# Performance work log

Measured on AMD Instinct MI355X. Metric: run time of the kernel, lower is better.

The kernel has to match this reference:

```python
import jax, jax.numpy as jnp
import numpy as np

V, E, H, L = 512, 128, 256, 4
B, T = 128, 1024


def setup_inputs() -> dict:
    key = jax.random.key(0)
    ks = jax.random.split(key, 16)
    s = 0.05
    inp = {
        "x": jax.random.randint(ks[0], (B, T), 0, V),
        "tags": jax.random.randint(ks[1], (B, T), 0, L),
        "mask": jnp.ones((B, T), dtype=bool),
        "emb": jax.random.normal(ks[2], (V, E), jnp.float32) * s,
        "w_ih_f": jax.random.normal(ks[3], (3 * H, E), jnp.float32) * s,
        "w_hh_f": jax.random.normal(ks[4], (3 * H, H), jnp.float32) * s,
        "b_ih_f": jax.random.normal(ks[5], (3 * H,), jnp.float32) * s,
        "b_hh_f": jax.random.normal(ks[6], (3 * H,), jnp.float32) * s,
        "w_ih_b": jax.random.normal(ks[7], (3 * H, E), jnp.float32) * s,
        "w_hh_b": jax.random.normal(ks[8], (3 * H, H), jnp.float32) * s,
        "b_ih_b": jax.random.normal(ks[9], (3 * H,), jnp.float32) * s,
        "b_hh_b": jax.random.normal(ks[10], (3 * H,), jnp.float32) * s,
        "fc_w": jax.random.normal(ks[11], (L, 2 * H), jnp.float32) * s,
        "fc_b": jax.random.normal(ks[12], (L,), jnp.float32) * s,
        "start_trans": jax.random.normal(ks[13], (L,), jnp.float32) * 0.1,
        "end_trans": jax.random.normal(ks[14], (L,), jnp.float32) * 0.1,
        "trans": jax.random.normal(ks[15], (L, L), jnp.float32) * 0.1,
    }
    return inp


def _gru_scan(xe, w_ih, w_hh, b_ih, b_hh):
    # xe: [B,T,E] -> out [B,T,H]; PyTorch GRU gate order: r, z, n
    gi = jnp.einsum("bte,ge->btg", xe, w_ih) + b_ih  # [B,T,3H]
    gi = jnp.swapaxes(gi, 0, 1)  # [T,B,3H]
    h0 = jnp.zeros((xe.shape[0], H), xe.dtype)

    def step(h, gi_t):
        gh = h @ w_hh.T + b_hh
        i_r, i_z, i_n = jnp.split(gi_t, 3, axis=-1)
        h_r, h_z, h_n = jnp.split(gh, 3, axis=-1)
        r = jax.nn.sigmoid(i_r + h_r)
        z = jax.nn.sigmoid(i_z + h_z)
        n = jnp.tanh(i_n + r * h_n)
        h_new = (1.0 - z) * n + z * h
        return h_new, h_new

    _, out = jax.lax.scan(step, h0, gi)
    return jnp.swapaxes(out, 0, 1)  # [B,T,H]


def _crf_neg_llh(emissions, tags, mask, start_trans, end_trans, trans):
    # emissions [B,T,L], tags [B,T] int, mask [B,T] bool
    maskf = mask.astype(emissions.dtype)
    # ----- numerator: score of gold path -----
    em_sel = jnp.take_along_axis(emissions, tags[..., None], axis=2)[..., 0]  # [B,T]
    trans_sel = trans[tags[:, :-1], tags[:, 1:]]  # [B,T-1]
    score = start_trans[tags[:, 0]] + em_sel[:, 0]
    score = score + jnp.sum((trans_sel + em_sel[:, 1:]) * maskf[:, 1:], axis=1)
    seq_ends = jnp.sum(mask.astype(jnp.int32), axis=1) - 1  # [B]
    last_tags = jnp.take_along_axis(tags, seq_ends[:, None], axis=1)[:, 0]
    score = score + end_trans[last_tags]
    # ----- denominator: forward algorithm (logsumexp scan) -----
    alpha0 = start_trans[None, :] + emissions[:, 0]  # [B,L]
    em_rest = jnp.swapaxes(emissions[:, 1:], 0, 1)  # [T-1,B,L]
    m_rest = jnp.swapaxes(mask[:, 1:], 0, 1)  # [T-1,B]

    def step(alpha, inputs):
        emit_t, m_t = inputs
        nxt = jax.nn.logsumexp(alpha[:, :, None] + trans[None] + emit_t[:, None, :], axis=1)
        alpha = jnp.where(m_t[:, None], nxt, alpha)
        return alpha, None

    alpha, _ = jax.lax.scan(step, alpha0, (em_rest, m_rest))
    logZ = jax.nn.logsumexp(alpha + end_trans[None, :], axis=1)  # [B]
    llh = score - logZ
    return -jnp.mean(llh)  # reduction='mean', negated in Segmenter.forward


def reference(x, tags, mask, emb, w_ih_f, w_hh_f, b_ih_f, b_hh_f,
              w_ih_b, w_hh_b, b_ih_b, b_hh_b, fc_w, fc_b,
              start_trans, end_trans, trans):
    xe = emb[x]  # [B,T,E]
    out_f = _gru_scan(xe, w_ih_f, w_hh_f, b_ih_f, b_hh_f)
    out_b = _gru_scan(xe[:, ::-1], w_ih_b, w_hh_b, b_ih_b, b_hh_b)[:, ::-1]
    gru_out = jnp.concatenate([out_f, out_b], axis=-1)  # [B,T,2H]
    emissions = jnp.einsum("bth,lh->btl", gru_out, fc_w) + fc_b  # [B,T,L]
    return _crf_neg_llh(emissions, tags, mask, start_trans, end_trans, trans)
```

## Files before the change

kernel.cpp:

```cpp
#include <hip/hip_runtime.h>
#include <hip/hip_fp16.h>

#define Tn 1024
#define NB 128
#define WPAD 260

typedef _Float16 h2_t __attribute__((ext_vector_type(2)));

__device__ __forceinline__ float dot2f(h2_t a, h2_t b, float c) {
#if __has_builtin(__builtin_amdgcn_fdot2)
  return __builtin_amdgcn_fdot2(a, b, c, false);
#else
  return c + (float)a[0] * (float)b[0] + (float)a[1] * (float)b[1];
#endif
}

__device__ __forceinline__ h2_t u2h(unsigned u) {
  union { unsigned u; h2_t h; } c; c.u = u; return c.h;
}

__global__ __launch_bounds__(768)
void gv_build(const float* __restrict__ emb,
              const float* __restrict__ wihf, const float* __restrict__ bihf,
              const float* __restrict__ wihb, const float* __restrict__ bihb,
              float* __restrict__ gv)
{
  const int d  = blockIdx.x >> 7;
  const int v4 = (blockIdx.x & 127) * 4;
  const float* wih = d ? wihb : wihf;
  const float* bih = d ? bihb : bihf;
  __shared__ float se[4][128];
  const int tid = threadIdx.x;
  if (tid < 512) se[tid >> 7][tid & 127] = emb[(v4 + (tid >> 7)) * 128 + (tid & 127)];
  __syncthreads();
  const int row = tid;
  const float b0 = bih[row];
  float a0 = b0, a1 = b0, a2 = b0, a3 = b0;
  #pragma unroll
  for (int e = 0; e < 128; e += 4) {
    const float4 w = *reinterpret_cast<const float4*>(&wih[row * 128 + e]);
    a0 = fmaf(w.x, se[0][e], a0); a0 = fmaf(w.y, se[0][e+1], a0);
    a0 = fmaf(w.z, se[0][e+2], a0); a0 = fmaf(w.w, se[0][e+3], a0);
    a1 = fmaf(w.x, se[1][e], a1); a1 = fmaf(w.y, se[1][e+1], a1);
    a1 = fmaf(w.z, se[1][e+2], a1); a1 = fmaf(w.w, se[1][e+3], a1);
    a2 = fmaf(w.x, se[2][e], a2); a2 = fmaf(w.y, se[2][e+1], a2);
    a2 = fmaf(w.z, se[2][e+2], a2); a2 = fmaf(w.w, se[2][e+3], a2);
    a3 = fmaf(w.x, se[3][e], a3); a3 = fmaf(w.y, se[3][e+1], a3);
    a3 = fmaf(w.z, se[3][e+2], a3); a3 = fmaf(w.w, se[3][e+3], a3);
  }
  float* out = gv + (size_t)(d * 512 + v4) * 768 + row;
  out[0] = a0; out[768] = a1; out[1536] = a2; out[2304] = a3;
}

__global__ __launch_bounds__(512, 2)
void gru_scan(const int* __restrict__ x,
              const float* __restrict__ gv,
              const float* __restrict__ whhf,
              const float* __restrict__ whhb,
              const float* __restrict__ bhhf,
              const float* __restrict__ bhhb,
              const float* __restrict__ fcw,
              float* __restrict__ em)
{
  const int tid  = threadIdx.x;
  const int j    = tid >> 1;
  const int half = tid & 1;
  const int dir  = blockIdx.x & 1;
  const int b    = blockIdx.x >> 1;

  const float* whh = dir ? whhb : whhf;
  const float* bhh = dir ? bhhb : bhhf;

  __shared__ float wstage[64 * WPAD];
  __shared__ __align__(16) _Float16 hbuf[2][256];

  h2_t wr[64], wz[64], wn[64];

  for (int ch = 0; ch < 12; ++ch) {
    const int r0 = ch * 64;
    #pragma unroll
    for (int i = 0; i < 8; ++i) {
      const int f  = (i * 512 + tid) * 4;
      const int rr = f >> 8;
      const int cc = f & 255;
      *reinterpret_cast<float4*>(&wstage[rr * WPAD + cc]) =
          *reinterpret_cast<const float4*>(&whh[(r0 + rr) * 256 + cc]);
    }
    __syncthreads();
    #pragma unroll
    for (int g = 0; g < 3; ++g) {
      const int row = j + g * 256;
      if (row >= r0 && row < r0 + 64) {
        const float* src = &wstage[(row - r0) * WPAD + half * 128];
        #pragma unroll
        for (int kk = 0; kk < 64; ++kk) {
          const float2 wv = *reinterpret_cast<const float2*>(&src[2 * kk]);
          h2_t w; w[0] = (_Float16)wv.x; w[1] = (_Float16)wv.y;
          if (g == 0) wr[kk] = w;
          else if (g == 1) wz[kk] = w;
          else wn[kk] = w;
        }
      }
    }
    __syncthreads();
  }

  float br = 0.f, bz = 0.f, bn = 0.f;
  if (half == 0) { br = bhh[j]; bz = bhh[j + 256]; bn = bhh[j + 512]; }

  const int el    = tid & 3;
  const int ec    = (tid >> 2) & 15;
  const int wv_id = tid >> 6;
  h2_t fc2[8];
  #pragma unroll
  for (int m = 0; m < 8; ++m) {
    const int cbase = el * 512 + dir * 256 + ec * 16 + 2 * m;
    fc2[m][0] = (_Float16)fcw[cbase];
    fc2[m][1] = (_Float16)fcw[cbase + 1];
  }

  if (tid < 256) hbuf[0][tid] = (_Float16)0.f;
  float ho = 0.f;
  __syncthreads();

  const int* xb  = x + b * Tn;
  float*     emo = em + (dir * NB + b) * Tn * 4;

  for (int step = 0; step < Tn; ++step) {
    const int cur = step & 1;
    const int tt  = dir ? (Tn - 1 - step) : step;

    const int tok = xb[tt];
    float gir = 0.f, giz = 0.f, gin = 0.f;
    if (half == 0) {
      const float* g = gv + (dir * 512 + tok) * 768;
      gir = g[j]; giz = g[j + 256]; gin = g[j + 512];
    }

    if (wv_id == (step & 7) && step > 0) {
      const int ptt = dir ? (Tn - step) : (step - 1);
      const uint4* hq4 = reinterpret_cast<const uint4*>(&hbuf[cur][0]) + ec * 2;
      const uint4 q0 = hq4[0];
      const uint4 q1 = hq4[1];
      float acc = 0.f;
      acc = dot2f(fc2[0], u2h(q0.x), acc);
      acc = dot2f(fc2[1], u2h(q0.y), acc);
      acc = dot2f(fc2[2], u2h(q0.z), acc);
      acc = dot2f(fc2[3], u2h(q0.w), acc);
      acc = dot2f(fc2[4], u2h(q1.x), acc);
      acc = dot2f(fc2[5], u2h(q1.y), acc);
      acc = dot2f(fc2[6], u2h(q1.z), acc);
      acc = dot2f(fc2[7], u2h(q1.w), acc);
      acc += __shfl_xor(acc, 4);
      acc += __shfl_xor(acc, 8);
      acc += __shfl_xor(acc, 16);
      acc += __shfl_xor(acc, 32);
      if (ec == 0) emo[ptt * 4 + el] = acc;
    }

    float dr = 0.f, dz = 0.f, dn = 0.f;
    const uint4* hv4 = reinterpret_cast<const uint4*>(&hbuf[cur][half * 128]);
    #pragma unroll
    for (int q = 0; q < 16; ++q) {
      const uint4 hq = hv4[q];
      const h2_t h0 = u2h(hq.x), h1 = u2h(hq.y), h2v = u2h(hq.z), h3 = u2h(hq.w);
      dr = dot2f(wr[4*q+0], h0, dr);  dz = dot2f(wz[4*q+0], h0, dz);  dn = dot2f(wn[4*q+0], h0, dn);
      dr = dot2f(wr[4*q+1], h1, dr);  dz = dot2f(wz[4*q+1], h1, dz);  dn = dot2f(wn[4*q+1], h1, dn);
      dr = dot2f(wr[4*q+2], h2v, dr); dz = dot2f(wz[4*q+2], h2v, dz); dn = dot2f(wn[4*q+2], h2v, dn);
      dr = dot2f(wr[4*q+3], h3, dr);  dz = dot2f(wz[4*q+3], h3, dz);  dn = dot2f(wn[4*q+3], h3, dn);
    }

    const float pr = __shfl_xor(dr, 1);
    const float pz = __shfl_xor(dz, 1);
    const float pn = __shfl_xor(dn, 1);

    if (half == 0) {
      const float ghr = dr + pr + br;
      const float ghz = dz + pz + bz;
      const float ghn = dn + pn + bn;
      const float r = 1.f / (1.f + __expf(-(gir + ghr)));
      const float z = 1.f / (1.f + __expf(-(giz + ghz)));
      const float npre = gin + r * ghn;
      const float e2 = __expf(-2.f * npre);
      const float n = (1.f - e2) / (1.f + e2);
      const float hnew = (1.f - z) * n + z * ho;
      ho = hnew;
      hbuf[cur ^ 1][j] = (_Float16)hnew;
    }
    __syncthreads();
  }

  if (wv_id == 0) {
    const int ptt = dir ? 0 : (Tn - 1);
    const uint4* hq4 = reinterpret_cast<const uint4*>(&hbuf[Tn & 1][0]) + ec * 2;
    const uint4 q0 = hq4[0];
    const uint4 q1 = hq4[1];
    float acc = 0.f;
    acc = dot2f(fc2[0], u2h(q0.x), acc);
    acc = dot2f(fc2[1], u2h(q0.y), acc);
    acc = dot2f(fc2[2], u2h(q0.z), acc);
    acc = dot2f(fc2[3], u2h(q0.w), acc);
    acc = dot2f(fc2[4], u2h(q1.x), acc);
    acc = dot2f(fc2[5], u2h(q1.y), acc);
    acc = dot2f(fc2[6], u2h(q1.z), acc);
    acc = dot2f(fc2[7], u2h(q1.w), acc);
    acc += __shfl_xor(acc, 4);
    acc += __shfl_xor(acc, 8);
    acc += __shfl_xor(acc, 16);
    acc += __shfl_xor(acc, 32);
    if (ec == 0) emo[ptt * 4 + el] = acc;
  }
}

__global__ __launch_bounds__(64)
void crf_nllh(const int* __restrict__ tags,
              const float* __restrict__ em,
              const float* __restrict__ fc_b,
              const float* __restrict__ st,
              const float* __restrict__ et,
              const float* __restrict__ tr,
              float* __restrict__ llh)
{
  const int lane = threadIdx.x;
  const int l = lane & 3;
  const int q = lane >> 2;
  const int b = blockIdx.x * 16 + q;
  const float* ef = em + (size_t)b * Tn * 4;
  const float* eb = em + ((size_t)NB + b) * Tn * 4;
  const int* tg = tags + b * Tn;
  const float fcb = fc_b[l];
  const float tc0 = tr[l * 4 + l];
  const float tc1 = tr[(l ^ 1) * 4 + l];
  const float tc2 = tr[(l ^ 2) * 4 + l];
  const float tc3 = tr[(l ^ 3) * 4 + l];

  const float e0 = ef[l] + eb[l] + fcb;
  float alpha = st[l] + e0;
  int tprev = tg[0];
  float score = (tprev == l) ? (st[l] + e0) : 0.f;

  #pragma unroll 8
  for (int t = 1; t < Tn; ++t) {
    const float e = ef[t * 4 + l] + eb[t * 4 + l] + fcb;
    const int tc = tg[t];
    if (tc == l) {
      const int s2 = tprev ^ l;
      const float tsel = (s2 & 1) ? ((s2 & 2) ? tc3 : tc1)
                                  : ((s2 & 2) ? tc2 : tc0);
      score += e + tsel;
    }
    tprev = tc;
    const float a1 = __shfl_xor(alpha, 1);
    const float a2 = __shfl_xor(alpha, 2);
    const float a3 = __shfl_xor(alpha, 3);
    const float v0 = alpha + tc0;
    const float v1 = a1 + tc1;
    const float v2 = a2 + tc2;
    const float v3 = a3 + tc3;
    const float mx = fmaxf(fmaxf(v0, v1), fmaxf(v2, v3));
    const float s = __expf(v0 - mx) + __expf(v1 - mx) + __expf(v2 - mx) + __expf(v3 - mx);
    alpha = mx + __logf(s) + e;
  }

  score += (tprev == l) ? et[l] : 0.f;
  float ae = alpha + et[l];
  float m1 = fmaxf(ae, __shfl_xor(ae, 1));
  m1 = fmaxf(m1, __shfl_xor(m1, 2));
  float se = __expf(ae - m1);
  se += __shfl_xor(se, 1);
  se += __shfl_xor(se, 2);
  const float logZ = m1 + __logf(se);
  float sc = score + __shfl_xor(score, 1);
  sc += __shfl_xor(sc, 2);
  if (l == 0) llh[b] = sc - logZ;
}

__global__ __launch_bounds__(128)
void reduce_mean(const float* __restrict__ llh, float* __restrict__ out)
{
  const int t = threadIdx.x;
  float v = llh[t];
  #pragma unroll
  for (int m = 32; m >= 1; m >>= 1) v += __shfl_xor(v, m);
  __shared__ float s2[2];
  if ((t & 63) == 0) s2[t >> 6] = v;
  __syncthreads();
  if (t == 0) out[0] = -(s2[0] + s2[1]) * (1.f / 128.f);
}

extern "C" void kernel_launch(void* const* d_in, const int* in_sizes, int n_in,
                              void* d_out, int out_size, void* d_ws, size_t ws_size,
                              hipStream_t stream) {
  const int*   x    = (const int*)d_in[0];
  const int*   tags = (const int*)d_in[1];
  const float* emb  = (const float*)d_in[3];
  const float* wihf = (const float*)d_in[4];
  const float* whhf = (const float*)d_in[5];
  const float* bihf = (const float*)d_in[6];
  const float* bhhf = (const float*)d_in[7];
  const float* wihb = (const float*)d_in[8];
  const float* whhb = (const float*)d_in[9];
  const float* bihb = (const float*)d_in[10];
  const float* bhhb = (const float*)d_in[11];
  const float* fcw  = (const float*)d_in[12];
  const float* fcb  = (const float*)d_in[13];
  const float* st   = (const float*)d_in[14];
  const float* et   = (const float*)d_in[15];
  const float* tr   = (const float*)d_in[16];

  char* ws = (char*)d_ws;
  float* gv  = (float*)ws;
  float* em  = (float*)(ws + 3145728);
  float* llh = (float*)(ws + 3145728 + 4194304);

  gv_build<<<dim3(256), dim3(768), 0, stream>>>(emb, wihf, bihf, wihb, bihb, gv);
  gru_scan<<<dim3(256), dim3(512), 0, stream>>>(x, gv, whhf, whhb, bhhf, bhhb, fcw, em);
  crf_nllh<<<dim3(8), dim3(64), 0, stream>>>(tags, em, fcb, st, et, tr, llh);
  reduce_mean<<<dim3(1), dim3(128), 0, stream>>>(llh, (float*)d_out);
}
```

Baseline: 1.512 ms.

## Split each GRU hidden unit across four lanes with 1024-thread blocks and DPP reductions

```diff
diff --git a/kernel.cpp b/kernel.cpp
--- a/kernel.cpp
+++ b/kernel.cpp
@@ -3,7 +3,6 @@
 
 #define Tn 1024
 #define NB 128
-#define WPAD 260
 
 typedef _Float16 h2_t __attribute__((ext_vector_type(2)));
 
@@ -17,6 +16,15 @@
 
 __device__ __forceinline__ h2_t u2h(unsigned u) {
   union { unsigned u; h2_t h; } c; c.u = u; return c.h;
+}
+
+__device__ __forceinline__ float dpp_xor1(float v) {
+  int i = __builtin_bit_cast(int, v);
+  return __builtin_bit_cast(float, __builtin_amdgcn_update_dpp(i, i, 0xB1, 0xF, 0xF, true));
+}
+__device__ __forceinline__ float dpp_xor2(float v) {
+  int i = __builtin_bit_cast(int, v);
+  return __builtin_bit_cast(float, __builtin_amdgcn_update_dpp(i, i, 0x4E, 0xF, 0xF, true));
 }
 
 __global__ __launch_bounds__(768)
@@ -52,7 +60,7 @@
   out[0] = a0; out[768] = a1; out[1536] = a2; out[2304] = a3;
 }
 
-__global__ __launch_bounds__(512, 2)
+__global__ __launch_bounds__(1024)
 void gru_scan(const int* __restrict__ x,
               const float* __restrict__ gv,
               const float* __restrict__ whhf,
@@ -62,95 +70,95 @@
               const float* __restrict__ fcw,
               float* __restrict__ em)
 {
-  const int tid  = threadIdx.x;
-  const int j    = tid >> 1;
-  const int half = tid & 1;
-  const int dir  = blockIdx.x & 1;
-  const int b    = blockIdx.x >> 1;
+  const int tid = threadIdx.x;
+  const int j   = tid >> 2;
+  const int q   = tid & 3;
+  const int dir = blockIdx.x & 1;
+  const int b   = blockIdx.x >> 1;
 
   const float* whh = dir ? whhb : whhf;
   const float* bhh = dir ? bhhb : bhhf;
 
-  __shared__ float wstage[64 * WPAD];
-  __shared__ __align__(16) _Float16 hbuf[2][256];
-
-  h2_t wr[64], wz[64], wn[64];
-
-  for (int ch = 0; ch < 12; ++ch) {
-    const int r0 = ch * 64;
+  __shared__ float wstage[128][260];
+  __shared__ __align__(16) char hb[2 * 576];
+  __shared__ __align__(16) h2_t fcs[4][132];
+
+  if (tid < 512) {
+    const int l = tid >> 7, c = tid & 127;
+    h2_t f;
+    f[0] = (_Float16)fcw[l * 512 + dir * 256 + 2 * c];
+    f[1] = (_Float16)fcw[l * 512 + dir * 256 + 2 * c + 1];
+    fcs[l][c] = f;
+  }
+  if (tid < 72) *reinterpret_cast<uint4*>(hb + tid * 16) = make_uint4(0, 0, 0, 0);
+
+  h2_t w[96];
+  for (int ch = 0; ch < 6; ++ch) {
+    const int r0 = ch << 7;
     #pragma unroll
     for (int i = 0; i < 8; ++i) {
-      const int f  = (i * 512 + tid) * 4;
-      const int rr = f >> 8;
-      const int cc = f & 255;
-      *reinterpret_cast<float4*>(&wstage[rr * WPAD + cc]) =
-          *reinterpret_cast<const float4*>(&whh[(r0 + rr) * 256 + cc]);
+      const int f  = i * 1024 + tid;
+      const int rr = f >> 6;
+      const int cc = (f & 63) << 2;
+      *reinterpret_cast<float4*>(&wstage[rr][cc]) =
+          *reinterpret_cast<const float4*>(&whh[(size_t)(r0 + rr) * 256 + cc]);
     }
     __syncthreads();
     #pragma unroll
     for (int g = 0; g < 3; ++g) {
-      const int row = j + g * 256;
-      if (row >= r0 && row < r0 + 64) {
-        const float* src = &wstage[(row - r0) * WPAD + half * 128];
+      const int row = (g << 8) + j;
+      if (row >= r0 && row < r0 + 128) {
+        const float* src = &wstage[row - r0][q << 6];
         #pragma unroll
-        for (int kk = 0; kk < 64; ++kk) {
-          const float2 wv = *reinterpret_cast<const float2*>(&src[2 * kk]);
-          h2_t w; w[0] = (_Float16)wv.x; w[1] = (_Float16)wv.y;
-          if (g == 0) wr[kk] = w;
-          else if (g == 1) wz[kk] = w;
-          else wn[kk] = w;
+        for (int kk = 0; kk < 32; ++kk) {
+          const float2 wv = *reinterpret_cast<const float2*>(src + 2 * kk);
+          h2_t ww; ww[0] = (_Float16)wv.x; ww[1] = (_Float16)wv.y;
+          w[(g << 5) + kk] = ww;
         }
       }
     }
     __syncthreads();
   }
 
-  float br = 0.f, bz = 0.f, bn = 0.f;
-  if (half == 0) { br = bhh[j]; bz = bhh[j + 256]; bn = bhh[j + 512]; }
-
-  const int el    = tid & 3;
-  const int ec    = (tid >> 2) & 15;
-  const int wv_id = tid >> 6;
-  h2_t fc2[8];
-  #pragma unroll
-  for (int m = 0; m < 8; ++m) {
-    const int cbase = el * 512 + dir * 256 + ec * 16 + 2 * m;
-    fc2[m][0] = (_Float16)fcw[cbase];
-    fc2[m][1] = (_Float16)fcw[cbase + 1];
-  }
-
-  if (tid < 256) hbuf[0][tid] = (_Float16)0.f;
-  float ho = 0.f;
-  __syncthreads();
-
-  const int* xb  = x + b * Tn;
-  float*     emo = em + (dir * NB + b) * Tn * 4;
+  float br = 0.f, bz = 0.f, bn = 0.f, ho = 0.f;
+  if (q == 0) { br = bhh[j]; bz = bhh[j + 256]; bn = bhh[j + 512]; }
+
+  const float* gvd  = gv + (size_t)dir * (512 * 768);
+  const int*   xb   = x + b * Tn;
+  float*       emo  = em + (size_t)(dir * NB + b) * (Tn * 4);
+  const int    wv_id = tid >> 6;
+  const int    el    = tid & 3;
+  const int    ec    = (tid >> 2) & 15;
+  const int    hq_off = q * 144;
+  const int    hw_off = (j >> 6) * 144 + (j & 63) * 2;
 
   for (int step = 0; step < Tn; ++step) {
     const int cur = step & 1;
     const int tt  = dir ? (Tn - 1 - step) : step;
-
     const int tok = xb[tt];
+
     float gir = 0.f, giz = 0.f, gin = 0.f;
-    if (half == 0) {
-      const float* g = gv + (dir * 512 + tok) * 768;
-      gir = g[j]; giz = g[j + 256]; gin = g[j + 512];
-    }
-
-    if (wv_id == (step & 7) && step > 0) {
+    if (q == 0) {
+      const float* g = gvd + tok * 768 + j;
+      gir = g[0]; giz = g[256]; gin = g[512];
+    }
+
+    if (wv_id == (step & 15) && step > 0) {
       const int ptt = dir ? (Tn - step) : (step - 1);
-      const uint4* hq4 = reinterpret_cast<const uint4*>(&hbuf[cur][0]) + ec * 2;
-      const uint4 q0 = hq4[0];
-      const uint4 q1 = hq4[1];
+      const char* hp = hb + cur * 576 + (ec >> 2) * 144 + (ec & 3) * 32;
+      const uint4 hA = *reinterpret_cast<const uint4*>(hp);
+      const uint4 hB = *reinterpret_cast<const uint4*>(hp + 16);
+      const uint4 fA = *reinterpret_cast<const uint4*>(&fcs[el][ec * 8]);
+      const uint4 fB = *reinterpret_cast<const uint4*>(&fcs[el][ec * 8 + 4]);
       float acc = 0.f;
-      acc = dot2f(fc2[0], u2h(q0.x), acc);
-      acc = dot2f(fc2[1], u2h(q0.y), acc);
-      acc = dot2f(fc2[2], u2h(q0.z), acc);
-      acc = dot2f(fc2[3], u2h(q0.w), acc);
-      acc = dot2f(fc2[4], u2h(q1.x), acc);
-      acc = dot2f(fc2[5], u2h(q1.y), acc);
-      acc = dot2f(fc2[6], u2h(q1.z), acc);
-      acc = dot2f(fc2[7], u2h(q1.w), acc);
+      acc = dot2f(u2h(fA.x), u2h(hA.x), acc);
+      acc = dot2f(u2h(fA.y), u2h(hA.y), acc);
+      acc = dot2f(u2h(fA.z), u2h(hA.z), acc);
+      acc = dot2f(u2h(fA.w), u2h(hA.w), acc);
+      acc = dot2f(u2h(fB.x), u2h(hB.x), acc);
+      acc = dot2f(u2h(fB.y), u2h(hB.y), acc);
+      acc = dot2f(u2h(fB.z), u2h(hB.z), acc);
+      acc = dot2f(u2h(fB.w), u2h(hB.w), acc);
       acc += __shfl_xor(acc, 4);
       acc += __shfl_xor(acc, 8);
       acc += __shfl_xor(acc, 16);
@@ -159,51 +167,50 @@
     }
 
     float dr = 0.f, dz = 0.f, dn = 0.f;
-    const uint4* hv4 = reinterpret_cast<const uint4*>(&hbuf[cur][half * 128]);
+    const char* hbase = hb + cur * 576 + hq_off;
     #pragma unroll
-    for (int q = 0; q < 16; ++q) {
-      const uint4 hq = hv4[q];
+    for (int c = 0; c < 8; ++c) {
+      const uint4 hq = *reinterpret_cast<const uint4*>(hbase + c * 16);
       const h2_t h0 = u2h(hq.x), h1 = u2h(hq.y), h2v = u2h(hq.z), h3 = u2h(hq.w);
-      dr = dot2f(wr[4*q+0], h0, dr);  dz = dot2f(wz[4*q+0], h0, dz);  dn = dot2f(wn[4*q+0], h0, dn);
-      dr = dot2f(wr[4*q+1], h1, dr);  dz = dot2f(wz[4*q+1], h1, dz);  dn = dot2f(wn[4*q+1], h1, dn);
-      dr = dot2f(wr[4*q+2], h2v, dr); dz = dot2f(wz[4*q+2], h2v, dz); dn = dot2f(wn[4*q+2], h2v, dn);
-      dr = dot2f(wr[4*q+3], h3, dr);  dz = dot2f(wz[4*q+3], h3, dz);  dn = dot2f(wn[4*q+3], h3, dn);
-    }
-
-    const float pr = __shfl_xor(dr, 1);
-    const float pz = __shfl_xor(dz, 1);
-    const float pn = __shfl_xor(dn, 1);
-
-    if (half == 0) {
-      const float ghr = dr + pr + br;
-      const float ghz = dz + pz + bz;
-      const float ghn = dn + pn + bn;
-      const float r = 1.f / (1.f + __expf(-(gir + ghr)));
-      const float z = 1.f / (1.f + __expf(-(giz + ghz)));
-      const float npre = gin + r * ghn;
-      const float e2 = __expf(-2.f * npre);
-      const float n = (1.f - e2) / (1.f + e2);
+      dr = dot2f(w[4*c+0], h0, dr);  dz = dot2f(w[32+4*c+0], h0, dz);  dn = dot2f(w[64+4*c+0], h0, dn);
+      dr = dot2f(w[4*c+1], h1, dr);  dz = dot2f(w[32+4*c+1], h1, dz);  dn = dot2f(w[64+4*c+1], h1, dn);
+      dr = dot2f(w[4*c+2], h2v, dr); dz = dot2f(w[32+4*c+2], h2v, dz); dn = dot2f(w[64+4*c+2], h2v, dn);
+      dr = dot2f(w[4*c+3], h3, dr);  dz = dot2f(w[32+4*c+3], h3, dz);  dn = dot2f(w[64+4*c+3], h3, dn);
+    }
+
+    dr += dpp_xor1(dr); dr += dpp_xor2(dr);
+    dz += dpp_xor1(dz); dz += dpp_xor2(dz);
+    dn += dpp_xor1(dn); dn += dpp_xor2(dn);
+
+    if (q == 0) {
+      const float r    = 1.f / (1.f + __expf(-(gir + dr + br)));
+      const float z    = 1.f / (1.f + __expf(-(giz + dz + bz)));
+      const float npre = gin + r * (dn + bn);
+      const float e2   = __expf(-2.f * npre);
+      const float n    = (1.f - e2) / (1.f + e2);
       const float hnew = (1.f - z) * n + z * ho;
       ho = hnew;
-      hbuf[cur ^ 1][j] = (_Float16)hnew;
+      *reinterpret_cast<_Float16*>(hb + (cur ^ 1) * 576 + hw_off) = (_Float16)hnew;
     }
     __syncthreads();
   }
 
   if (wv_id == 0) {
     const int ptt = dir ? 0 : (Tn - 1);
-    const uint4* hq4 = reinterpret_cast<const uint4*>(&hbuf[Tn & 1][0]) + ec * 2;
-    const uint4 q0 = hq4[0];
-    const uint4 q1 = hq4[1];
+    const char* hp = hb + (Tn & 1) * 576 + (ec >> 2) * 144 + (ec & 3) * 32;
+    const uint4 hA = *reinterpret_cast<const uint4*>(hp);
+    const uint4 hB = *reinterpret_cast<const uint4*>(hp + 16);
+    const uint4 fA = *reinterpret_cast<const uint4*>(&fcs[el][ec * 8]);
+    const uint4 fB = *reinterpret_cast<const uint4*>(&fcs[el][ec * 8 + 4]);
     float acc = 0.f;
-    acc = dot2f(fc2[0], u2h(q0.x), acc);
-    acc = dot2f(fc2[1], u2h(q0.y), acc);
-    acc = dot2f(fc2[2], u2h(q0.z), acc);
-    acc = dot2f(fc2[3], u2h(q0.w), acc);
-    acc = dot2f(fc2[4], u2h(q1.x), acc);
-    acc = dot2f(fc2[5], u2h(q1.y), acc);
-    acc = dot2f(fc2[6], u2h(q1.z), acc);
-    acc = dot2f(fc2[7], u2h(q1.w), acc);
+    acc = dot2f(u2h(fA.x), u2h(hA.x), acc);
+    acc = dot2f(u2h(fA.y), u2h(hA.y), acc);
+    acc = dot2f(u2h(fA.z), u2h(hA.z), acc);
+    acc = dot2f(u2h(fA.w), u2h(hA.w), acc);
+    acc = dot2f(u2h(fB.x), u2h(hB.x), acc);
+    acc = dot2f(u2h(fB.y), u2h(hB.y), acc);
+    acc = dot2f(u2h(fB.z), u2h(hB.z), acc);
+    acc = dot2f(u2h(fB.w), u2h(hB.w), acc);
     acc += __shfl_xor(acc, 4);
     acc += __shfl_xor(acc, 8);
     acc += __shfl_xor(acc, 16);
@@ -314,7 +321,7 @@
   float* llh = (float*)(ws + 3145728 + 4194304);
 
   gv_build<<<dim3(256), dim3(768), 0, stream>>>(emb, wihf, bihf, wihb, bihb, gv);
-  gru_scan<<<dim3(256), dim3(512), 0, stream>>>(x, gv, whhf, whhb, bhhf, bhhb, fcw, em);
+  gru_scan<<<dim3(256), dim3(1024), 0, stream>>>(x, gv, whhf, whhb, bhhf, bhhb, fcw, em);
   crf_nllh<<<dim3(8), dim3(64), 0, stream>>>(tags, em, fcb, st, et, tr, llh);
   reduce_mean<<<dim3(1), dim3(128), 0, stream>>>(llh, (float*)d_out);
 }
```

New measurement: 2.256 ms. 1.49x slower.

## Batch 16 sequences per block and compute GRU recurrence with MFMA

Applied to the files above, without the earlier changes.

```diff
diff --git a/kernel.cpp b/kernel.cpp
--- a/kernel.cpp
+++ b/kernel.cpp
@@ -3,37 +3,30 @@
 
 #define Tn 1024
 #define NB 128
-#define WPAD 260
-
-typedef _Float16 h2_t __attribute__((ext_vector_type(2)));
-
-__device__ __forceinline__ float dot2f(h2_t a, h2_t b, float c) {
-#if __has_builtin(__builtin_amdgcn_fdot2)
-  return __builtin_amdgcn_fdot2(a, b, c, false);
-#else
-  return c + (float)a[0] * (float)b[0] + (float)a[1] * (float)b[1];
-#endif
-}
-
-__device__ __forceinline__ h2_t u2h(unsigned u) {
-  union { unsigned u; h2_t h; } c; c.u = u; return c.h;
-}
+
+#define S_RZ (-1.4426950408889634f)
+#define S_N  (-2.8853900817779268f)
+
+typedef _Float16 f16x8 __attribute__((ext_vector_type(8)));
+typedef _Float16 f16x4 __attribute__((ext_vector_type(4)));
+typedef float    f32x4 __attribute__((ext_vector_type(4)));
 
 __global__ __launch_bounds__(768)
 void gv_build(const float* __restrict__ emb,
-              const float* __restrict__ wihf, const float* __restrict__ bihf,
-              const float* __restrict__ wihb, const float* __restrict__ bihb,
-              float* __restrict__ gv)
+              const float* __restrict__ wihf, const float* __restrict__ bihf, const float* __restrict__ bhhf,
+              const float* __restrict__ wihb, const float* __restrict__ bihb, const float* __restrict__ bhhb,
+              _Float16* __restrict__ gv2)
 {
   const int d  = blockIdx.x >> 7;
   const int v4 = (blockIdx.x & 127) * 4;
   const float* wih = d ? wihb : wihf;
   const float* bih = d ? bihb : bihf;
+  const float* bhh = d ? bhhb : bhhf;
   __shared__ float se[4][128];
   const int tid = threadIdx.x;
   if (tid < 512) se[tid >> 7][tid & 127] = emb[(v4 + (tid >> 7)) * 128 + (tid & 127)];
   __syncthreads();
-  const int row = tid;
+  const int row = tid, g = row >> 8, j = row & 255;
   const float b0 = bih[row];
   float a0 = b0, a1 = b0, a2 = b0, a3 = b0;
   #pragma unroll
@@ -48,167 +41,163 @@
     a3 = fmaf(w.x, se[3][e], a3); a3 = fmaf(w.y, se[3][e+1], a3);
     a3 = fmaf(w.z, se[3][e+2], a3); a3 = fmaf(w.w, se[3][e+3], a3);
   }
-  float* out = gv + (size_t)(d * 512 + v4) * 768 + row;
-  out[0] = a0; out[768] = a1; out[1536] = a2; out[2304] = a3;
+  const float sc  = (g == 2) ? S_N : S_RZ;
+  const float add = (g < 2) ? bhh[row] : 0.f;
+  _Float16* base = gv2 + ((size_t)(d * 512 + v4) * 64 + (j >> 2)) * 16 + g * 4 + (j & 3);
+  base[0]    = (_Float16)(sc * (a0 + add));
+  base[1024] = (_Float16)(sc * (a1 + add));
+  base[2048] = (_Float16)(sc * (a2 + add));
+  base[3072] = (_Float16)(sc * (a3 + add));
+  if (g == 2) {
+    const _Float16 bv = (_Float16)(S_N * bhh[row]);
+    _Float16* bb = gv2 + ((size_t)(d * 512 + v4) * 64 + (j >> 2)) * 16 + 12 + (j & 3);
+    bb[0] = bv; bb[1024] = bv; bb[2048] = bv; bb[3072] = bv;
+  }
 }
 
 __global__ __launch_bounds__(512, 2)
 void gru_scan(const int* __restrict__ x,
-              const float* __restrict__ gv,
+              const _Float16* __restrict__ gv2,
               const float* __restrict__ whhf,
               const float* __restrict__ whhb,
-              const float* __restrict__ bhhf,
-              const float* __restrict__ bhhb,
               const float* __restrict__ fcw,
               float* __restrict__ em)
 {
-  const int tid  = threadIdx.x;
-  const int j    = tid >> 1;
-  const int half = tid & 1;
-  const int dir  = blockIdx.x & 1;
-  const int b    = blockIdx.x >> 1;
+  const int tid = threadIdx.x;
+  const int w   = tid >> 6;
+  const int l   = tid & 63;
+  const int m   = l & 15;
+  const int q   = l >> 4;
+  const int dir = blockIdx.x & 1;
+  const int b0  = (blockIdx.x >> 1) * 16;
 
   const float* whh = dir ? whhb : whhf;
-  const float* bhh = dir ? bhhb : bhhf;
-
-  __shared__ float wstage[64 * WPAD];
-  __shared__ __align__(16) _Float16 hbuf[2][256];
-
-  h2_t wr[64], wz[64], wn[64];
-
-  for (int ch = 0; ch < 12; ++ch) {
-    const int r0 = ch * 64;
-    #pragma unroll
-    for (int i = 0; i < 8; ++i) {
-      const int f  = (i * 512 + tid) * 4;
-      const int rr = f >> 8;
-      const int cc = f & 255;
-      *reinterpret_cast<float4*>(&wstage[rr * WPAD + cc]) =
-          *reinterpret_cast<const float4*>(&whh[(r0 + rr) * 256 + cc]);
+
+  __shared__ _Float16 hls[2][16][264];
+  __shared__ _Float16 emf[8][512];
+
+  for (int i = tid; i < 2 * 16 * 264; i += 512) (&hls[0][0][0])[i] = (_Float16)0.f;
+
+  if (w == 7) {
+    #pragma unroll
+    for (int ks = 0; ks < 8; ++ks) {
+      f16x8 f;
+      #pragma unroll
+      for (int e = 0; e < 8; ++e) {
+        float v = (m < 4) ? fcw[m * 512 + dir * 256 + ks * 32 + q * 8 + e] : 0.f;
+        f[e] = (_Float16)v;
+      }
+      *reinterpret_cast<f16x8*>(&emf[ks][l * 8]) = f;
+    }
+  }
+
+  f16x8 af[2][3][8];
+  #pragma unroll
+  for (int blk = 0; blk < 2; ++blk) {
+    #pragma unroll
+    for (int g = 0; g < 3; ++g) {
+      const int row = g * 256 + (w + 8 * blk) * 16 + m;
+      const float sc = (g == 2) ? S_N : S_RZ;
+      const float* wrow = whh + (size_t)row * 256 + q * 8;
+      #pragma unroll
+      for (int ks = 0; ks < 8; ++ks) {
+        const float4 c0 = *reinterpret_cast<const float4*>(wrow + ks * 32);
+        const float4 c1 = *reinterpret_cast<const float4*>(wrow + ks * 32 + 4);
+        f16x8 f;
+        f[0] = (_Float16)(c0.x * sc); f[1] = (_Float16)(c0.y * sc);
+        f[2] = (_Float16)(c0.z * sc); f[3] = (_Float16)(c0.w * sc);
+        f[4] = (_Float16)(c1.x * sc); f[5] = (_Float16)(c1.y * sc);
+        f[6] = (_Float16)(c1.z * sc); f[7] = (_Float16)(c1.w * sc);
+        af[blk][g][ks] = f;
+      }
+    }
+  }
+  __syncthreads();
+
+  const int*      xrow = x + (size_t)(b0 + m) * Tn;
+  const _Float16* gvd  = gv2 + (size_t)dir * 512 * 1024;
+  float*          emo  = em + (size_t)(dir * NB + b0 + m) * (Tn * 4);
+
+  int tok = xrow[dir ? (Tn - 1) : 0];
+
+  for (int t = 0; t < Tn; ++t) {
+    const int cur = t & 1;
+    const _Float16* hc = &hls[cur][0][0];
+    _Float16*       hn = &hls[cur ^ 1][0][0];
+
+    const _Float16* gp0 = gvd + (size_t)tok * 1024 + ((w + 0) * 4 + q) * 16;
+    const _Float16* gp1 = gvd + (size_t)tok * 1024 + ((w + 8) * 4 + q) * 16;
+    const f16x8 rz0 = *reinterpret_cast<const f16x8*>(gp0);
+    const f16x8 nb0 = *reinterpret_cast<const f16x8*>(gp0 + 8);
+    const f16x8 rz1 = *reinterpret_cast<const f16x8*>(gp1);
+    const f16x8 nb1 = *reinterpret_cast<const f16x8*>(gp1 + 8);
+    if (t + 1 < Tn) tok = xrow[dir ? (Tn - 2 - t) : (t + 1)];
+
+    const f16x4 ho0 = *reinterpret_cast<const f16x4*>(hc + m * 264 + (w + 0) * 16 + q * 4);
+    const f16x4 ho1 = *reinterpret_cast<const f16x4*>(hc + m * 264 + (w + 8) * 16 + q * 4);
+
+    f32x4 acc[2][3] = {{{0,0,0,0},{0,0,0,0},{0,0,0,0}},{{0,0,0,0},{0,0,0,0},{0,0,0,0}}};
+    f32x4 acce = {0,0,0,0};
+    #pragma unroll
+    for (int ks = 0; ks < 8; ++ks) {
+      const f16x8 b = *reinterpret_cast<const f16x8*>(hc + m * 264 + ks * 32 + q * 8);
+      #pragma unroll
+      for (int blk = 0; blk < 2; ++blk) {
+        acc[blk][0] = __builtin_amdgcn_mfma_f32_16x16x32_f16(af[blk][0][ks], b, acc[blk][0], 0, 0, 0);
+        acc[blk][1] = __builtin_amdgcn_mfma_f32_16x16x32_f16(af[blk][1][ks], b, acc[blk][1], 0, 0, 0);
+        acc[blk][2] = __builtin_amdgcn_mfma_f32_16x16x32_f16(af[blk][2][ks], b, acc[blk][2], 0, 0, 0);
+      }
+      if (w == 7) {
+        const f16x8 ef = *reinterpret_cast<const f16x8*>(&emf[ks][l * 8]);
+        acce = __builtin_amdgcn_mfma_f32_16x16x32_f16(ef, b, acce, 0, 0, 0);
+      }
+    }
+
+    if (w == 7 && t > 0 && l < 16) {
+      const int ptt = dir ? (Tn - t) : (t - 1);
+      *reinterpret_cast<f32x4*>(emo + (size_t)ptt * 4) = acce;
+    }
+
+    #pragma unroll
+    for (int blk = 0; blk < 2; ++blk) {
+      const f16x8 rzv = blk ? rz1 : rz0;
+      const f16x8 nbv = blk ? nb1 : nb0;
+      const f16x4 hov = blk ? ho1 : ho0;
+      f16x4 hnv;
+      #pragma unroll
+      for (int r4 = 0; r4 < 4; ++r4) {
+        const float aR = acc[blk][0][r4], aZ = acc[blk][1][r4], aN = acc[blk][2][r4];
+        const float pr = aR + (float)rzv[r4];
+        const float er = __builtin_amdgcn_exp2f(pr);
+        const float rr = __builtin_amdgcn_rcpf(1.f + er);
+        const float pz = aZ + (float)rzv[4 + r4];
+        const float ez = __builtin_amdgcn_exp2f(pz);
+        const float zz = __builtin_amdgcn_rcpf(1.f + ez);
+        float y = fmaf(rr, aN + (float)nbv[4 + r4], (float)nbv[r4]);
+        y = fminf(y, 60.f);
+        const float en = __builtin_amdgcn_exp2f(y);
+        const float nn = (1.f - en) * __builtin_amdgcn_rcpf(1.f + en);
+        const float hv = fmaf(zz, (float)hov[r4] - nn, nn);
+        hnv[r4] = (_Float16)hv;
+      }
+      *reinterpret_cast<f16x4*>(hn + m * 264 + (w + 8 * blk) * 16 + q * 4) = hnv;
     }
     __syncthreads();
-    #pragma unroll
-    for (int g = 0; g < 3; ++g) {
-      const int row = j + g * 256;
-      if (row >= r0 && row < r0 + 64) {
-        const float* src = &wstage[(row - r0) * WPAD + half * 128];
-        #pragma unroll
-        for (int kk = 0; kk < 64; ++kk) {
-          const float2 wv = *reinterpret_cast<const float2*>(&src[2 * kk]);
-          h2_t w; w[0] = (_Float16)wv.x; w[1] = (_Float16)wv.y;
-          if (g == 0) wr[kk] = w;
-          else if (g == 1) wz[kk] = w;
-          else wn[kk] = w;
-        }
-      }
-    }
-    __syncthreads();
-  }
-
-  float br = 0.f, bz = 0.f, bn = 0.f;
-  if (half == 0) { br = bhh[j]; bz = bhh[j + 256]; bn = bhh[j + 512]; }
-
-  const int el    = tid & 3;
-  const int ec    = (tid >> 2) & 15;
-  const int wv_id = tid >> 6;
-  h2_t fc2[8];
-  #pragma unroll
-  for (int m = 0; m < 8; ++m) {
-    const int cbase = el * 512 + dir * 256 + ec * 16 + 2 * m;
-    fc2[m][0] = (_Float16)fcw[cbase];
-    fc2[m][1] = (_Float16)fcw[cbase + 1];
-  }
-
-  if (tid < 256) hbuf[0][tid] = (_Float16)0.f;
-  float ho = 0.f;
-  __syncthreads();
-
-  const int* xb  = x + b * Tn;
-  float*     emo = em + (dir * NB + b) * Tn * 4;
-
-  for (int step = 0; step < Tn; ++step) {
-    const int cur = step & 1;
-    const int tt  = dir ? (Tn - 1 - step) : step;
-
-    const int tok = xb[tt];
-    float gir = 0.f, giz = 0.f, gin = 0.f;
-    if (half == 0) {
-      const float* g = gv + (dir * 512 + tok) * 768;
-      gir = g[j]; giz = g[j + 256]; gin = g[j + 512];
-    }
-
-    if (wv_id == (step & 7) && step > 0) {
-      const int ptt = dir ? (Tn - step) : (step - 1);
-      const uint4* hq4 = reinterpret_cast<const uint4*>(&hbuf[cur][0]) + ec * 2;
-      const uint4 q0 = hq4[0];
-      const uint4 q1 = hq4[1];
-      float acc = 0.f;
-      acc = dot2f(fc2[0], u2h(q0.x), acc);
-      acc = dot2f(fc2[1], u2h(q0.y), acc);
-      acc = dot2f(fc2[2], u2h(q0.z), acc);
-      acc = dot2f(fc2[3], u2h(q0.w), acc);
-      acc = dot2f(fc2[4], u2h(q1.x), acc);
-      acc = dot2f(fc2[5], u2h(q1.y), acc);
-      acc = dot2f(fc2[6], u2h(q1.z), acc);
-      acc = dot2f(fc2[7], u2h(q1.w), acc);
-      acc += __shfl_xor(acc, 4);
-      acc += __shfl_xor(acc, 8);
-      acc += __shfl_xor(acc, 16);
-      acc += __shfl_xor(acc, 32);
-      if (ec == 0) emo[ptt * 4 + el] = acc;
-    }
-
-    float dr = 0.f, dz = 0.f, dn = 0.f;
-    const uint4* hv4 = reinterpret_cast<const uint4*>(&hbuf[cur][half * 128]);
-    #pragma unroll
-    for (int q = 0; q < 16; ++q) {
-      const uint4 hq = hv4[q];
-      const h2_t h0 = u2h(hq.x), h1 = u2h(hq.y), h2v = u2h(hq.z), h3 = u2h(hq.w);
-      dr = dot2f(wr[4*q+0], h0, dr);  dz = dot2f(wz[4*q+0], h0, dz);  dn = dot2f(wn[4*q+0], h0, dn);
-      dr = dot2f(wr[4*q+1], h1, dr);  dz = dot2f(wz[4*q+1], h1, dz);  dn = dot2f(wn[4*q+1], h1, dn);
-      dr = dot2f(wr[4*q+2], h2v, dr); dz = dot2f(wz[4*q+2], h2v, dz); dn = dot2f(wn[4*q+2], h2v, dn);
-      dr = dot2f(wr[4*q+3], h3, dr);  dz = dot2f(wz[4*q+3], h3, dz);  dn = dot2f(wn[4*q+3], h3, dn);
-    }
-
-    const float pr = __shfl_xor(dr, 1);
-    const float pz = __shfl_xor(dz, 1);
-    const float pn = __shfl_xor(dn, 1);
-
-    if (half == 0) {
-      const float ghr = dr + pr + br;
-      const float ghz = dz + pz + bz;
-      const float ghn = dn + pn + bn;
-      const float r = 1.f / (1.f + __expf(-(gir + ghr)));
-      const float z = 1.f / (1.f + __expf(-(giz + ghz)));
-      const float npre = gin + r * ghn;
-      const float e2 = __expf(-2.f * npre);
-      const float n = (1.f - e2) / (1.f + e2);
-      const float hnew = (1.f - z) * n + z * ho;
-      ho = hnew;
-      hbuf[cur ^ 1][j] = (_Float16)hnew;
-    }
-    __syncthreads();
-  }
-
-  if (wv_id == 0) {
-    const int ptt = dir ? 0 : (Tn - 1);
-    const uint4* hq4 = reinterpret_cast<const uint4*>(&hbuf[Tn & 1][0]) + ec * 2;
-    const uint4 q0 = hq4[0];
-    const uint4 q1 = hq4[1];
-    float acc = 0.f;
-    acc = dot2f(fc2[0], u2h(q0.x), acc);
-    acc = dot2f(fc2[1], u2h(q0.y), acc);
-    acc = dot2f(fc2[2], u2h(q0.z), acc);
-    acc = dot2f(fc2[3], u2h(q0.w), acc);
-    acc = dot2f(fc2[4], u2h(q1.x), acc);
-    acc = dot2f(fc2[5], u2h(q1.y), acc);
-    acc = dot2f(fc2[6], u2h(q1.z), acc);
-    acc = dot2f(fc2[7], u2h(q1.w), acc);
-    acc += __shfl_xor(acc, 4);
-    acc += __shfl_xor(acc, 8);
-    acc += __shfl_xor(acc, 16);
-    acc += __shfl_xor(acc, 32);
-    if (ec == 0) emo[ptt * 4 + el] = acc;
+  }
+
+  if (w == 7) {
+    const _Float16* hc = &hls[Tn & 1][0][0];
+    f32x4 acce = {0,0,0,0};
+    #pragma unroll
+    for (int ks = 0; ks < 8; ++ks) {
+      const f16x8 b  = *reinterpret_cast<const f16x8*>(hc + m * 264 + ks * 32 + q * 8);
+      const f16x8 ef = *reinterpret_cast<const f16x8*>(&emf[ks][l * 8]);
+      acce = __builtin_amdgcn_mfma_f32_16x16x32_f16(ef, b, acce, 0, 0, 0);
+    }
+    if (l < 16) {
+      const int ptt = dir ? 0 : (Tn - 1);
+      *reinterpret_cast<f32x4*>(emo + (size_t)ptt * 4) = acce;
+    }
   }
 }
 
@@ -309,12 +298,12 @@
   const float* tr   = (const float*)d_in[16];
 
   char* ws = (char*)d_ws;
-  float* gv  = (float*)ws;
-  float* em  = (float*)(ws + 3145728);
-  float* llh = (float*)(ws + 3145728 + 4194304);
-
-  gv_build<<<dim3(256), dim3(768), 0, stream>>>(emb, wihf, bihf, wihb, bihb, gv);
-  gru_scan<<<dim3(256), dim3(512), 0, stream>>>(x, gv, whhf, whhb, bhhf, bhhb, fcw, em);
+  _Float16* gv2 = (_Float16*)ws;
+  float*    em  = (float*)(ws + 2097152);
+  float*    llh = (float*)(ws + 2097152 + 4194304);
+
+  gv_build<<<dim3(256), dim3(768), 0, stream>>>(emb, wihf, bihf, bhhf, wihb, bihb, bhhb, gv2);
+  gru_scan<<<dim3(16), dim3(512), 0, stream>>>(x, gv2, whhf, whhb, fcw, em);
   crf_nllh<<<dim3(8), dim3(64), 0, stream>>>(tags, em, fcb, st, et, tr, llh);
   reduce_mean<<<dim3(1), dim3(128), 0, stream>>>(llh, (float*)d_out);
 }
```

Measured after the change: 3.868 ms. 2.56x slower.
